# Kernel tuning notes

Measured on AMD Instinct MI355X. Metric: run time of the kernel, lower is better.

The kernel has to match this reference:

```python
import jax, jax.numpy as jnp
import numpy as np

D = 256      # embedding_dim
K = 1024     # num_embeddings
B, S = 32, 2048

def setup_inputs() -> dict:
    key = jax.random.key(0)
    k1, k2 = jax.random.split(key)
    inp = jax.random.normal(k1, (B, S, D), dtype=jnp.float32)
    w = jax.random.normal(k2, (D, K), dtype=jnp.float32)  # codebook, [D, K]
    return {"input": inp, "w": w, "weights_loss": 0}


def reference(input, w, weights_loss):
    # flatten tokens: [N, D]
    flat = input.reshape(-1, D)
    N = flat.shape[0]
    # squared euclidean distances to each code: [N, K]
    distances = (jnp.sum(flat * flat, axis=1, keepdims=True)
                 - 2.0 * (flat @ w)
                 + jnp.sum(w * w, axis=0, keepdims=True))
    # nearest code per token (argmax of -dist == argmin of dist)
    flat_idx = jnp.argmax(-distances, axis=1)              # [N] int
    idx = flat_idx.reshape(input.shape[:-1])               # [B, S]
    # embedding gather: w.T is [K, D]
    quantize = jnp.take(w.T, idx, axis=0)                  # [B, S, D]
    # commitment loss: mse(stop_grad(quantize), flat_input)
    q_flat = quantize.reshape(-1, D)
    loss = jnp.mean((jax.lax.stop_gradient(q_flat) - flat) ** 2)
    # straight-through estimator
    quantize_st = input + jax.lax.stop_gradient(quantize - input)
    # one-hot statistics without materializing [N, K]
    dema_cluster_size = jax.ops.segment_sum(
        jnp.ones((N,), dtype=flat.dtype), flat_idx, num_segments=K)  # [K]
    dw = jax.ops.segment_sum(flat, flat_idx, num_segments=K).T       # [D, K]
    avg_probs = dema_cluster_size / N
    perplexity = jnp.exp(-jnp.sum(avg_probs * jnp.log(avg_probs + 1e-10)))
    return (loss,
            quantize_st,
            dema_cluster_size.reshape(1, K),
            dw.reshape(1, D, K),
            idx,
            perplexity)
```

## Files before the change

kernel.cpp:

```cpp
#include <hip/hip_runtime.h>


#define D 256
#define K 1024
#define NTOK 65536

#define OFF_Q   ((size_t)1)
#define OFF_CS  ((size_t)1 + (size_t)NTOK * D)
#define OFF_DW  (OFF_CS + K)
#define OFF_IDX (OFF_DW + (size_t)D * K)
#define OFF_P   (OFF_IDX + NTOK)

#define FLAG_TH  0.05f
#define FLAG_CAP 8192

typedef __attribute__((ext_vector_type(8))) short short8;
typedef __attribute__((ext_vector_type(16))) float f32x16;

__device__ __forceinline__ unsigned short f2bf(float f) {
  unsigned u = __float_as_uint(f);
  return (unsigned short)((u + 0x7FFFu + ((u >> 16) & 1u)) >> 16);
}
__device__ __forceinline__ float bf2f(unsigned short h) {
  return __uint_as_float(((unsigned)h) << 16);
}

__device__ __forceinline__ void gload_lds16(void* g, void* l) {
  __builtin_amdgcn_global_load_lds(
      (__attribute__((address_space(1))) unsigned int*)g,
      (__attribute__((address_space(3))) unsigned int*)l, 16, 0, 0);
}

__global__ __launch_bounds__(256) void prep_w(const float* __restrict__ w,
                                              float* __restrict__ wT,
                                              unsigned short* __restrict__ wBG) {
  __shared__ float tile[32][33];
  const int k0 = blockIdx.x * 32, d0 = blockIdx.y * 32;
  const int tx = threadIdx.x, ty = threadIdx.y;
#pragma unroll
  for (int j = 0; j < 4; ++j) {
    const int r = ty + j * 8;
    tile[r][tx] = w[(size_t)(d0 + r) * K + k0 + tx];
  }
  __syncthreads();
#pragma unroll
  for (int j = 0; j < 4; ++j) {
    const int r = ty + j * 8;
    const int k = k0 + r, d = d0 + tx;
    const float v = tile[tx][r];
    wT[(size_t)k * D + d] = v;
    const unsigned short h = f2bf(v);
    const unsigned short l = f2bf(v - bf2f(h));
    const size_t frag = (size_t)(((d >> 4) * 2 + ((d >> 3) & 1)) * 32 + (k & 31)) * 8 +
                        (d & 7);
    const size_t base = (size_t)(k >> 5) * 16384;
    wBG[base + frag] = h;
    wBG[base + 8192 + frag] = l;
  }
}

__global__ __launch_bounds__(256) void wsq_kernel(const float* __restrict__ wT,
                                                  float* __restrict__ wsq) {
  const int wave = threadIdx.x >> 6, lane = threadIdx.x & 63;
  const int k = blockIdx.x * 4 + wave;
  const float4 v = *(const float4*)(wT + (size_t)k * D + lane * 4);
  float s = v.x * v.x + v.y * v.y + v.z * v.z + v.w * v.w;
#pragma unroll
  for (int m = 1; m < 64; m <<= 1) s += __shfl_xor(s, m);
  if (lane == 0) wsq[k] = s;
}

__global__ __launch_bounds__(256, 2) void vq_score(
    const float* __restrict__ x, unsigned short* __restrict__ wBG,
    const float* __restrict__ wsq, const float* __restrict__ wT,
    float* __restrict__ out, int* __restrict__ idxInt, int* __restrict__ countsInt,
    int* __restrict__ flagCnt, int* __restrict__ flagged) {
  __shared__ short sB[2][16384];
  __shared__ float swsq[K];

  const int tid = threadIdx.x;
#pragma unroll
  for (int j = 0; j < 4; ++j) swsq[tid + j * 256] = wsq[tid + j * 256];

  const int wv = tid >> 6, lane = tid & 63;
  const int col = lane & 31, hi = lane >> 5;
  const int rowG = blockIdx.x * 128 + wv * 32 + col;

  auto stage = [&](int chunk, int buf) {
    unsigned short* src = wBG + (size_t)chunk * 16384 + wv * 4096 + lane * 8;
    short* dst = &sB[buf][wv * 4096];
#pragma unroll
    for (int j = 0; j < 8; ++j)
      gload_lds16(src + j * 512, dst + j * 512);
  };

  stage(0, 0);

  short8 ah[16], al[16];
  {
    const float* xr = x + (size_t)rowG * D + hi * 8;
#pragma unroll
    for (int s = 0; s < 16; ++s) {
      const float4 f0 = *(const float4*)(xr + s * 16);
      const float4 f1 = *(const float4*)(xr + s * 16 + 4);
      const float fv[8] = {f0.x, f0.y, f0.z, f0.w, f1.x, f1.y, f1.z, f1.w};
      short8 a, b;
#pragma unroll
      for (int e = 0; e < 8; ++e) {
        const unsigned short h = f2bf(fv[e]);
        a[e] = (short)h;
        b[e] = (short)f2bf(fv[e] - bf2f(h));
      }
      ah[s] = a;
      al[s] = b;
    }
  }

  float s1[16], s2[16];
  int i1[16];
#pragma unroll
  for (int r = 0; r < 16; ++r) { s1[r] = -3.4e38f; s2[r] = -3.4e38f; i1[r] = 0; }

  __syncthreads();

  for (int chunk = 0; chunk < 32; ++chunk) {
    const int cur = chunk & 1;
    if (chunk + 1 < 32) stage(chunk + 1, cur ^ 1);

    const short* bhB = sB[cur];
    const short* blB = sB[cur] + 8192;
    f32x16 ahh, ahl, alh;
#pragma unroll
    for (int r = 0; r < 16; ++r) { ahh[r] = 0.f; ahl[r] = 0.f; alh[r] = 0.f; }
#pragma unroll
    for (int s = 0; s < 16; ++s) {
      const int off = ((s * 2 + hi) << 8) + (col << 3);
      const short8 bh = *(const short8*)(bhB + off);
      const short8 bl = *(const short8*)(blB + off);
      ahh = __builtin_amdgcn_mfma_f32_32x32x16_bf16(ah[s], bh, ahh, 0, 0, 0);
      ahl = __builtin_amdgcn_mfma_f32_32x32x16_bf16(ah[s], bl, ahl, 0, 0, 0);
      alh = __builtin_amdgcn_mfma_f32_32x32x16_bf16(al[s], bh, alh, 0, 0, 0);
    }

    const int cc = chunk * 32 + col;
    const float wq = swsq[cc];
#pragma unroll
    for (int r = 0; r < 16; ++r) {
      const float sc = fmaf(2.f, ahh[r] + ahl[r] + alh[r], -wq);
      const bool gt = sc > s1[r];
      s2[r] = fmaxf(s2[r], gt ? s1[r] : sc);
      if (gt) { s1[r] = sc; i1[r] = cc; }
    }
    __syncthreads();
  }

#pragma unroll
  for (int m = 1; m <= 16; m <<= 1) {
#pragma unroll
    for (int r = 0; r < 16; ++r) {
      const float os1 = __shfl_xor(s1[r], m);
      const int   oi1 = __shfl_xor(i1[r], m);
      const float os2 = __shfl_xor(s2[r], m);
      const bool take = (os1 > s1[r]) || (os1 == s1[r] && oi1 < i1[r]);
      const float loser = take ? s1[r] : os1;
      if (take) { s1[r] = os1; i1[r] = oi1; }
      s2[r] = fmaxf(fmaxf(s2[r], os2), loser);
    }
  }

  const size_t tb = (size_t)blockIdx.x * 128 + wv * 32;

  if (col == 0) {
#pragma unroll
    for (int r = 0; r < 16; ++r) {
      const int row = (r & 3) + 8 * (r >> 2) + 4 * hi;
      const size_t g = tb + row;
      idxInt[g] = i1[r];
      out[OFF_IDX + g] = (float)i1[r];
      atomicAdd(countsInt + i1[r], 1);
      if (s1[r] - s2[r] < FLAG_TH) {
        const int slot = atomicAdd(flagCnt, 1);
        if (slot < FLAG_CAP) flagged[slot] = (int)g;
      }
    }
  }

  const int l32 = lane & 31;
#pragma unroll
  for (int r = 0; r < 16; ++r) {
    const int row = (r & 3) + 8 * (r >> 2) + 4 * hi;
    const size_t t = tb + row;
    const int k = i1[r];
    const float* wrow = wT + (size_t)k * D + l32 * 8;
    const float4 q0 = *(const float4*)(wrow);
    const float4 q1 = *(const float4*)(wrow + 4);
    float* od = out + OFF_Q + t * D + l32 * 8;
    od[0] = q0.x; od[1] = q0.y; od[2] = q0.z; od[3] = q0.w;
    od[4] = q1.x; od[5] = q1.y; od[6] = q1.z; od[7] = q1.w;
  }
}

__global__ __launch_bounds__(256) void vq_fixup(
    const float* __restrict__ x, const float* __restrict__ wT,
    const float* __restrict__ wsq, const int* __restrict__ flagCnt,
    const int* __restrict__ flagged, unsigned long long* __restrict__ keyBuf) {
  __shared__ float ws32[32 * 264];
  __shared__ float xs[D];
  __shared__ unsigned long long wred[4];
  const int tid = threadIdx.x;
  const int cc = blockIdx.x & 31, j0 = blockIdx.x >> 5;
#pragma unroll
  for (int r = 0; r < 32; ++r)
    ws32[r * 264 + tid] = wT[(size_t)(cc * 32 + r) * D + tid];
  int F = *flagCnt;
  if (F > FLAG_CAP) F = FLAG_CAP;
  const int ci = tid >> 3, dg = tid & 7, c = cc * 32 + ci;
  const float wq = wsq[c];

  for (int slot = j0; slot < F; slot += 16) {
    const int t = flagged[slot];
    __syncthreads();
    xs[tid] = x[(size_t)t * D + tid];
    __syncthreads();
    float dot = 0.f;
#pragma unroll
    for (int i = 0; i < 32; ++i)
      dot = fmaf(xs[dg + 8 * i], ws32[ci * 264 + dg + 8 * i], dot);
    dot += __shfl_xor(dot, 1);
    dot += __shfl_xor(dot, 2);
    dot += __shfl_xor(dot, 4);
    unsigned long long key = 0ull;
    if (dg == 0) {
      const float sc = fmaf(2.f, dot, -wq);
      unsigned u = __float_as_uint(sc);
      u = (u & 0x80000000u) ? ~u : (u | 0x80000000u);
      key = ((unsigned long long)u << 32) | (unsigned)(1023 - c);
    }
#pragma unroll
    for (int m = 8; m <= 32; m <<= 1) {
      const unsigned long long o = __shfl_xor(key, m);
      if (o > key) key = o;
    }
    if ((tid & 63) == 0) wred[tid >> 6] = key;
    __syncthreads();
    if (tid == 0) {
      unsigned long long b = wred[0];
      if (wred[1] > b) b = wred[1];
      if (wred[2] > b) b = wred[2];
      if (wred[3] > b) b = wred[3];
      keyBuf[(size_t)slot * 32 + cc] = b;
    }
  }
}

__global__ __launch_bounds__(256) void vq_fixfin(
    const int* __restrict__ flagCnt, const int* __restrict__ flagged,
    const unsigned long long* __restrict__ keyBuf, int* __restrict__ idxInt,
    int* __restrict__ countsInt, const float* __restrict__ wT,
    float* __restrict__ out) {
  int F = *flagCnt;
  if (F > FLAG_CAP) F = FLAG_CAP;
  const int wv = threadIdx.x >> 6, lane = threadIdx.x & 63;
  for (int slot = blockIdx.x * 4 + wv; slot < F; slot += 64) {
    const int t = flagged[slot];
    unsigned long long key = (lane < 32) ? keyBuf[(size_t)slot * 32 + lane] : 0ull;
#pragma unroll
    for (int m = 1; m <= 32; m <<= 1) {
      const unsigned long long o = __shfl_xor(key, m);
      if (o > key) key = o;
    }
    const int c = 1023 - (int)(key & 0xFFFFFFFFull);
    const int old = idxInt[t];
    if (c != old) {
      if (lane == 0) {
        idxInt[t] = c;
        out[OFF_IDX + t] = (float)c;
        atomicAdd(countsInt + old, -1);
        atomicAdd(countsInt + c, 1);
      }
      const float4 q = *(const float4*)(wT + (size_t)c * D + lane * 4);
      float* od = out + OFF_Q + (size_t)t * D + lane * 4;
      od[0] = q.x; od[1] = q.y; od[2] = q.z; od[3] = q.w;
    }
  }
}

__global__ __launch_bounds__(1024) void vq_scan(const int* __restrict__ countsInt,
                                                int* __restrict__ bucketStart,
                                                int* __restrict__ cursorInt,
                                                float* __restrict__ out) {
  __shared__ int sc[1024];
  const int tid = threadIdx.x;
  const int c = countsInt[tid];
  out[OFF_CS + tid] = (float)c;
  sc[tid] = c;
  __syncthreads();
  for (int off = 1; off < 1024; off <<= 1) {
    int v = 0;
    if (tid >= off) v = sc[tid - off];
    __syncthreads();
    if (tid >= off) sc[tid] += v;
    __syncthreads();
  }
  bucketStart[tid] = sc[tid] - c;
  cursorInt[tid] = 0;
}

__global__ __launch_bounds__(256) void vq_scatter(const int* __restrict__ idxInt,
                                                  const int* __restrict__ bucketStart,
                                                  int* __restrict__ cursorInt,
                                                  int* __restrict__ sortedTok) {
  const int t = blockIdx.x * 256 + threadIdx.x;
  const int k = idxInt[t];
  const int pos = atomicAdd(cursorInt + k, 1);
  sortedTok[bucketStart[k] + pos] = t;
}

__global__ __launch_bounds__(256) void vq_dwloss(
    const float* __restrict__ x, const float* __restrict__ wT,
    const int* __restrict__ idxInt, const int* __restrict__ sortedTok,
    float* __restrict__ dwT, float* __restrict__ lossAcc) {
  __shared__ float sRed[4];
  const int tid = threadIdx.x, wv = tid >> 6, lane = tid & 63;
  const int g = blockIdx.x * 4 + wv;
  const int p0 = g * 16;
  const int tk = sortedTok[p0 + (lane & 15)];
  const int kk = idxInt[tk];

  int kcur = -1;
  float4 acc = {0.f, 0.f, 0.f, 0.f};
  float4 wv4 = {0.f, 0.f, 0.f, 0.f};
  float lp = 0.f;
#pragma unroll
  for (int i = 0; i < 16; ++i) {
    const int t = __shfl(tk, i);
    const int k = __shfl(kk, i);
    if (k != kcur) {
      if (kcur >= 0) {
        float* dr = dwT + (size_t)kcur * D + lane * 4;
        atomicAdd(dr + 0, acc.x); atomicAdd(dr + 1, acc.y);
        atomicAdd(dr + 2, acc.z); atomicAdd(dr + 3, acc.w);
      }
      acc = {0.f, 0.f, 0.f, 0.f};
      wv4 = *(const float4*)(wT + (size_t)k * D + lane * 4);
      kcur = k;
    }
    const float4 xv = *(const float4*)(x + (size_t)t * D + lane * 4);
    acc.x += xv.x; acc.y += xv.y; acc.z += xv.z; acc.w += xv.w;
    const float dx = wv4.x - xv.x, dy = wv4.y - xv.y;
    const float dz = wv4.z - xv.z, dw = wv4.w - xv.w;
    lp = fmaf(dx, dx, lp); lp = fmaf(dy, dy, lp);
    lp = fmaf(dz, dz, lp); lp = fmaf(dw, dw, lp);
  }
  {
    float* dr = dwT + (size_t)kcur * D + lane * 4;
    atomicAdd(dr + 0, acc.x); atomicAdd(dr + 1, acc.y);
    atomicAdd(dr + 2, acc.z); atomicAdd(dr + 3, acc.w);
  }
#pragma unroll
  for (int m = 1; m < 64; m <<= 1) lp += __shfl_xor(lp, m);
  if (lane == 0) sRed[wv] = lp;
  __syncthreads();
  if (tid == 0) atomicAdd(lossAcc, sRed[0] + sRed[1] + sRed[2] + sRed[3]);
}

__global__ __launch_bounds__(256) void transpose_dw(const float* __restrict__ dwT,
                                                    float* __restrict__ out) {
  __shared__ float tile[32][33];
  const int d0 = blockIdx.x * 32, k0 = blockIdx.y * 32;
  const int tx = threadIdx.x, ty = threadIdx.y;
#pragma unroll
  for (int j = 0; j < 4; ++j) {
    const int r = ty + j * 8;
    tile[r][tx] = dwT[(size_t)(k0 + r) * D + d0 + tx];
  }
  __syncthreads();
#pragma unroll
  for (int j = 0; j < 4; ++j) {
    const int r = ty + j * 8;
    out[OFF_DW + (size_t)(d0 + r) * K + k0 + tx] = tile[tx][r];
  }
}

__global__ __launch_bounds__(1024) void finalize_kernel(const float* __restrict__ lossAcc,
                                                        float* __restrict__ out) {
  __shared__ float red[16];
  const int tid = threadIdx.x;
  const float c = out[OFF_CS + tid];
  const float avg = c * (1.0f / (float)NTOK);
  float term = avg * logf(avg + 1e-10f);
#pragma unroll
  for (int m = 1; m < 64; m <<= 1) term += __shfl_xor(term, m);
  const int wave = tid >> 6, lane = tid & 63;
  if (lane == 0) red[wave] = term;
  __syncthreads();
  if (tid == 0) {
    float s = 0.f;
#pragma unroll
    for (int i = 0; i < 16; ++i) s += red[i];
    out[OFF_P] = expf(-s);
    out[0] = lossAcc[0] * (1.0f / ((float)NTOK * (float)D));
  }
}

extern "C" void kernel_launch(void* const* d_in, const int* in_sizes, int n_in,
                              void* d_out, int out_size, void* d_ws, size_t ws_size,
                              hipStream_t stream) {
  const float* x = (const float*)d_in[0];
  const float* w = (const float*)d_in[1];
  float* out = (float*)d_out;
  char* wsb = (char*)d_ws;

  float* lossAcc     = (float*)(wsb + 0);
  int*   flagCnt     = (int*)(wsb + 4);
  int*   countsInt   = (int*)(wsb + 4096);
  int*   bucketStart = (int*)(wsb + 8192);
  int*   cursorInt   = (int*)(wsb + 12288);
  float* wsq         = (float*)(wsb + 16384);
  int*   idxInt      = (int*)(wsb + 20480);
  int*   sortedTok   = (int*)(wsb + 282624);
  int*   flagged     = (int*)(wsb + 544768);
  unsigned long long* keyBuf = (unsigned long long*)(wsb + 577536);
  float* wT          = (float*)(wsb + 2674688);
  unsigned short* wBG = (unsigned short*)(wsb + 3723264);
  float* dwT         = (float*)(wsb + 4771840);

  hipMemsetAsync(wsb, 0, 20480, stream);
  hipMemsetAsync(dwT, 0, sizeof(float) * (size_t)K * D, stream);

  prep_w<<<dim3(K / 32, D / 32), dim3(32, 8), 0, stream>>>(w, wT, wBG);
  wsq_kernel<<<dim3(K / 4), dim3(256), 0, stream>>>(wT, wsq);
  vq_score<<<dim3(NTOK / 128), dim3(256), 0, stream>>>(
      x, wBG, wsq, wT, out, idxInt, countsInt, flagCnt, flagged);
  vq_fixup<<<dim3(512), dim3(256), 0, stream>>>(x, wT, wsq, flagCnt, flagged, keyBuf);
  vq_fixfin<<<dim3(16), dim3(256), 0, stream>>>(flagCnt, flagged, keyBuf, idxInt,
                                                countsInt, wT, out);
  vq_scan<<<dim3(1), dim3(1024), 0, stream>>>(countsInt, bucketStart, cursorInt, out);
  vq_scatter<<<dim3(NTOK / 256), dim3(256), 0, stream>>>(idxInt, bucketStart,
                                                         cursorInt, sortedTok);
  vq_dwloss<<<dim3(1024), dim3(256), 0, stream>>>(x, wT, idxInt, sortedTok,
                                                  dwT, lossAcc);
  transpose_dw<<<dim3(D / 32, K / 32), dim3(32, 8), 0, stream>>>(dwT, out);
  finalize_kernel<<<dim3(1), dim3(1024), 0, stream>>>(lossAcc, out);
}
```

Baseline: 387.2 us.

## Read codebook fragments directly from global, tighten fixup threshold, widen fixup grid

The vq_score kernel no longer double-buffers codebook chunks in LDS through global_load_lds. Each lane now reads its bf16 B fragments straight from global memory, relying on L2/L1 caching, and the per-chunk barrier is removed. The quantize gather now uses lane-strided scalar copies instead of float4 loads. The near-tie flag threshold is tightened, which should flag fewer tokens for exact fp32 re-scoring, and the fixup kernel gets four times more blocks with a matching slot stride. The tighter threshold could miss ties that the split-bf16 scores fail to order correctly, and dropping LDS staging puts more load on the cache path.

```diff
diff --git a/kernel.cpp b/kernel.cpp
--- a/kernel.cpp
+++ b/kernel.cpp
@@ -11,7 +11,7 @@
 #define OFF_IDX (OFF_DW + (size_t)D * K)
 #define OFF_P   (OFF_IDX + NTOK)
 
-#define FLAG_TH  0.05f
+#define FLAG_TH  0.008f
 #define FLAG_CAP 8192
 
 typedef __attribute__((ext_vector_type(8))) short short8;
@@ -23,12 +23,6 @@
 }
 __device__ __forceinline__ float bf2f(unsigned short h) {
   return __uint_as_float(((unsigned)h) << 16);
-}
-
-__device__ __forceinline__ void gload_lds16(void* g, void* l) {
-  __builtin_amdgcn_global_load_lds(
-      (__attribute__((address_space(1))) unsigned int*)g,
-      (__attribute__((address_space(3))) unsigned int*)l, 16, 0, 0);
 }
 
 __global__ __launch_bounds__(256) void prep_w(const float* __restrict__ w,
@@ -71,11 +65,10 @@
 }
 
 __global__ __launch_bounds__(256, 2) void vq_score(
-    const float* __restrict__ x, unsigned short* __restrict__ wBG,
+    const float* __restrict__ x, const unsigned short* __restrict__ wBG,
     const float* __restrict__ wsq, const float* __restrict__ wT,
     float* __restrict__ out, int* __restrict__ idxInt, int* __restrict__ countsInt,
     int* __restrict__ flagCnt, int* __restrict__ flagged) {
-  __shared__ short sB[2][16384];
   __shared__ float swsq[K];
 
   const int tid = threadIdx.x;
@@ -85,16 +78,6 @@
   const int wv = tid >> 6, lane = tid & 63;
   const int col = lane & 31, hi = lane >> 5;
   const int rowG = blockIdx.x * 128 + wv * 32 + col;
-
-  auto stage = [&](int chunk, int buf) {
-    unsigned short* src = wBG + (size_t)chunk * 16384 + wv * 4096 + lane * 8;
-    short* dst = &sB[buf][wv * 4096];
-#pragma unroll
-    for (int j = 0; j < 8; ++j)
-      gload_lds16(src + j * 512, dst + j * 512);
-  };
-
-  stage(0, 0);
 
   short8 ah[16], al[16];
   {
@@ -124,19 +107,16 @@
   __syncthreads();
 
   for (int chunk = 0; chunk < 32; ++chunk) {
-    const int cur = chunk & 1;
-    if (chunk + 1 < 32) stage(chunk + 1, cur ^ 1);
-
-    const short* bhB = sB[cur];
-    const short* blB = sB[cur] + 8192;
+    const short8* bhG = (const short8*)(wBG + (size_t)chunk * 16384) + lane;
+    const short8* blG = bhG + 1024;
+
     f32x16 ahh, ahl, alh;
 #pragma unroll
     for (int r = 0; r < 16; ++r) { ahh[r] = 0.f; ahl[r] = 0.f; alh[r] = 0.f; }
 #pragma unroll
     for (int s = 0; s < 16; ++s) {
-      const int off = ((s * 2 + hi) << 8) + (col << 3);
-      const short8 bh = *(const short8*)(bhB + off);
-      const short8 bl = *(const short8*)(blB + off);
+      const short8 bh = bhG[s * 64];
+      const short8 bl = blG[s * 64];
       ahh = __builtin_amdgcn_mfma_f32_32x32x16_bf16(ah[s], bh, ahh, 0, 0, 0);
       ahl = __builtin_amdgcn_mfma_f32_32x32x16_bf16(ah[s], bl, ahl, 0, 0, 0);
       alh = __builtin_amdgcn_mfma_f32_32x32x16_bf16(al[s], bh, alh, 0, 0, 0);
@@ -151,7 +131,6 @@
       s2[r] = fmaxf(s2[r], gt ? s1[r] : sc);
       if (gt) { s1[r] = sc; i1[r] = cc; }
     }
-    __syncthreads();
   }
 
 #pragma unroll
@@ -191,12 +170,13 @@
     const int row = (r & 3) + 8 * (r >> 2) + 4 * hi;
     const size_t t = tb + row;
     const int k = i1[r];
-    const float* wrow = wT + (size_t)k * D + l32 * 8;
-    const float4 q0 = *(const float4*)(wrow);
-    const float4 q1 = *(const float4*)(wrow + 4);
-    float* od = out + OFF_Q + t * D + l32 * 8;
-    od[0] = q0.x; od[1] = q0.y; od[2] = q0.z; od[3] = q0.w;
-    od[4] = q1.x; od[5] = q1.y; od[6] = q1.z; od[7] = q1.w;
+    const float* wrow = wT + (size_t)k * D;
+    float* od = out + OFF_Q + t * D;
+#pragma unroll
+    for (int c = 0; c < 8; ++c) {
+      const int e = c * 32 + l32;
+      od[e] = wrow[e];
+    }
   }
 }
 
@@ -217,7 +197,7 @@
   const int ci = tid >> 3, dg = tid & 7, c = cc * 32 + ci;
   const float wq = wsq[c];
 
-  for (int slot = j0; slot < F; slot += 16) {
+  for (int slot = j0; slot < F; slot += 64) {
     const int t = flagged[slot];
     __syncthreads();
     xs[tid] = x[(size_t)t * D + tid];
@@ -432,7 +412,7 @@
   wsq_kernel<<<dim3(K / 4), dim3(256), 0, stream>>>(wT, wsq);
   vq_score<<<dim3(NTOK / 128), dim3(256), 0, stream>>>(
       x, wBG, wsq, wT, out, idxInt, countsInt, flagCnt, flagged);
-  vq_fixup<<<dim3(512), dim3(256), 0, stream>>>(x, wT, wsq, flagCnt, flagged, keyBuf);
+  vq_fixup<<<dim3(2048), dim3(256), 0, stream>>>(x, wT, wsq, flagCnt, flagged, keyBuf);
   vq_fixfin<<<dim3(16), dim3(256), 0, stream>>>(flagCnt, flagged, keyBuf, idxInt,
                                                 countsInt, wT, out);
   vq_scan<<<dim3(1), dim3(1024), 0, stream>>>(countsInt, bucketStart, cursorInt, out);
```

Measured after the change: 528.5 us. +36.5%, slower.
